# Kernel tuning notes

Measured on AMD Instinct MI355X. Metric: run time of the kernel, lower is better.

The kernel has to match this reference:

```python
import jax, jax.numpy as jnp
import numpy as np

C, H_HEADS, L_LEV, M_PTS = 256, 4, 3, 4
TAU0 = 1.0


def _ln(x, g, b, eps=1e-5):
    mu = x.mean(-1, keepdims=True)
    var = ((x - mu) ** 2).mean(-1, keepdims=True)
    return (x - mu) * jax.lax.rsqrt(var + eps) * g + b


def _grid_sample(v, grid):
    """Bilinear grid_sample, padding_mode='zeros', align_corners=True.
    v: [B,C,Hin,Win], grid: [B,N,2] (x,y) in [-1,1] -> [B,N,C]"""
    B, Cc, Hin, Win = v.shape
    x = (grid[..., 0] + 1.0) * 0.5 * (Win - 1)
    y = (grid[..., 1] + 1.0) * 0.5 * (Hin - 1)
    x0 = jnp.floor(x); y0 = jnp.floor(y)
    wx1 = x - x0; wy1 = y - y0
    x0i = x0.astype(jnp.int32); y0i = y0.astype(jnp.int32)
    vflat = v.reshape(B, Cc, Hin * Win).transpose(0, 2, 1)  # [B,HW,C]

    def tap(yi, xi, w):
        valid = ((xi >= 0) & (xi < Win) & (yi >= 0) & (yi < Hin)).astype(v.dtype)
        idx = jnp.clip(yi, 0, Hin - 1) * Win + jnp.clip(xi, 0, Win - 1)  # [B,N]
        g = jax.vmap(lambda vf, i: vf[i])(vflat, idx)  # [B,N,C]
        return g * (w * valid)[..., None]

    return (tap(y0i, x0i, (1 - wy1) * (1 - wx1))
            + tap(y0i, x0i + 1, (1 - wy1) * wx1)
            + tap(y0i + 1, x0i, wy1 * (1 - wx1))
            + tap(y0i + 1, x0i + 1, wy1 * wx1))


def setup_inputs() -> dict:
    key = jax.random.key(0)
    ks = jax.random.split(key, 32)
    B, Hq, Wq = 2, 64, 64
    cins = [256, 512, 1024]
    d = {
        'S':  jax.random.normal(ks[0], (B, C, Hq, Wq), jnp.float32),
        'f0': jax.random.normal(ks[1], (B, cins[0], 64, 64), jnp.float32),
        'f1': jax.random.normal(ks[2], (B, cins[1], 32, 32), jnp.float32),
        'f2': jax.random.normal(ks[3], (B, cins[2], 16, 16), jnp.float32),
        'sim': jax.random.uniform(ks[4], (B, 1, Hq, Wq), jnp.float32),
        # 1x1 conv value projections per level
        'vw0': jax.random.normal(ks[5], (C, cins[0]), jnp.float32) * 0.02,
        'vb0': jnp.zeros((C,), jnp.float32),
        'vw1': jax.random.normal(ks[6], (C, cins[1]), jnp.float32) * 0.02,
        'vb1': jnp.zeros((C,), jnp.float32),
        'vw2': jax.random.normal(ks[7], (C, cins[2]), jnp.float32) * 0.02,
        'vb2': jnp.zeros((C,), jnp.float32),
        'q_w': jax.random.normal(ks[8], (C, C), jnp.float32) * 0.02,
        'q_b': jnp.zeros((C,), jnp.float32),
        # offset/weight predictors (non-zero so sampling is nontrivial)
        'off_w': jax.random.normal(ks[9], (H_HEADS * L_LEV * M_PTS * 2, C), jnp.float32) * 0.01,
        'off_b': jnp.zeros((H_HEADS * L_LEV * M_PTS * 2,), jnp.float32),
        'wgt_w': jax.random.normal(ks[10], (H_HEADS * L_LEV * M_PTS, C), jnp.float32) * 0.02,
        'wgt_b': jnp.zeros((H_HEADS * L_LEV * M_PTS,), jnp.float32),
        'out_w': jax.random.normal(ks[11], (C, H_HEADS * C), jnp.float32) * 0.02,
        'out_b': jnp.zeros((C,), jnp.float32),
        'lnq_g': jnp.ones((C,), jnp.float32), 'lnq_b': jnp.zeros((C,), jnp.float32),
        'lno_g': jnp.ones((C,), jnp.float32), 'lno_b': jnp.zeros((C,), jnp.float32),
        'fc1_w': jax.random.normal(ks[12], (4 * C, C), jnp.float32) * 0.02,
        'fc1_b': jnp.zeros((4 * C,), jnp.float32),
        'fc2_w': jax.random.normal(ks[13], (C, 4 * C), jnp.float32) * 0.02,
        'fc2_b': jnp.zeros((C,), jnp.float32),
    }
    return d


def reference(S, f0, f1, f2, sim, vw0, vb0, vw1, vb1, vw2, vb2, q_w, q_b,
              off_w, off_b, wgt_w, wgt_b, out_w, out_b,
              lnq_g, lnq_b, lno_g, lno_b, fc1_w, fc1_b, fc2_w, fc2_b):
    B, Cc, Hq, Wq = S.shape
    Nq = Hq * Wq
    S_seq = S.reshape(B, Cc, Nq).transpose(0, 2, 1)  # [B,Nq,C]
    Q = _ln(S_seq @ q_w.T + q_b, lnq_g, lnq_b)

    # reference points in [0,1], (x,y)
    ys = jnp.linspace(0.5 / Hq, 1 - 0.5 / Hq, Hq)
    xs = jnp.linspace(0.5 / Wq, 1 - 0.5 / Wq, Wq)
    yy, xx = jnp.meshgrid(ys, xs, indexing='ij')
    ref = jnp.stack([xx, yy], axis=-1).reshape(1, Nq, 2)

    feats = [(f0, vw0, vb0), (f1, vw1, vb1), (f2, vw2, vb2)]
    V = [jnp.einsum('bchw,oc->bohw', f, w) + b[None, :, None, None] for f, w, b in feats]

    off = (Q @ off_w.T + off_b).reshape(B, Nq, H_HEADS, L_LEV, M_PTS, 2)
    wts = (Q @ wgt_w.T + wgt_b).reshape(B, Nq, H_HEADS, L_LEV, M_PTS)

    sim2 = sim[:, 0].reshape(B, Nq, 1)
    tau = TAU0 / (sim2 + 0.001)
    wts = wts / tau.reshape(B, Nq, 1, 1, 1)
    wts = jax.nn.softmax(wts.reshape(B, Nq, H_HEADS, L_LEV * M_PTS), axis=-1)
    wts = wts.reshape(B, Nq, H_HEADS, L_LEV, M_PTS)

    acc = jnp.zeros((B, Nq, H_HEADS, Cc), S.dtype)
    for l in range(L_LEV):
        g01 = ref.reshape(1, Nq, 1, 1, 2) + off[:, :, :, l]  # [B,Nq,H,M,2]
        g = jnp.clip(jnp.tanh(g01 * 2.0 - 1.0), -1.0, 1.0)
        samp = _grid_sample(V[l], g.reshape(B, Nq * H_HEADS * M_PTS, 2))
        samp = samp.reshape(B, Nq, H_HEADS, M_PTS, Cc)
        acc = acc + jnp.einsum('bqhmc,bqhm->bqhc', samp, wts[:, :, :, l])

    Y = acc.reshape(B, Nq, H_HEADS * Cc) @ out_w.T + out_b
    Z = _ln(S_seq + Y, lno_g, lno_b)
    h = jax.nn.gelu(Z @ fc1_w.T + fc1_b, approximate=False)
    Z = Z + (h @ fc2_w.T + fc2_b)
    return Z.transpose(0, 2, 1).reshape(B, Cc, Hq, Wq)
```

## Files before the change

kernel.cpp:

```cpp
#include <hip/hip_runtime.h>
#include <hip/hip_bf16.h>
#include <math.h>

#define NQ 4096
#define CC 256

typedef __attribute__((ext_vector_type(8))) short bfrag;
typedef __attribute__((ext_vector_type(4))) float ffrag;

__device__ inline unsigned short f2bf(float x) {
  __hip_bfloat16 h = __float2bfloat16(x);
  return *reinterpret_cast<unsigned short*>(&h);
}

__device__ inline float bf2f(unsigned short u) {
  return __uint_as_float(((unsigned)u) << 16);
}

__device__ inline void gload16(const void* g, void* l) {
  __builtin_amdgcn_global_load_lds(
      (const __attribute__((address_space(1))) void*)g,
      (__attribute__((address_space(3))) void*)l, 16, 0, 0);
}

__device__ void tr64(const float* __restrict__ src,
                     unsigned short* __restrict__ dstb, int Cin, int P,
                     int p0, int c0, int b, float (*t)[73]) {
  int tid = threadIdx.x;
  int rx = tid & 15, ry = tid >> 4;
  const float* Sb = src + (size_t)b * Cin * P + p0 + rx * 4;
  #pragma unroll
  for (int i = 0; i < 4; i++) {
    int r = ry + i * 16;
    float4 v = *(const float4*)(Sb + (size_t)(c0 + r) * P);
    t[r][rx * 4 + 0] = v.x; t[r][rx * 4 + 1] = v.y;
    t[r][rx * 4 + 2] = v.z; t[r][rx * 4 + 3] = v.w;
  }
  __syncthreads();
  size_t ob = (size_t)b * P * Cin;
  #pragma unroll
  for (int i = 0; i < 4; i++) {
    int pr = ry + i * 16;
    float x0 = t[rx * 4 + 0][pr], x1 = t[rx * 4 + 1][pr];
    float x2 = t[rx * 4 + 2][pr], x3 = t[rx * 4 + 3][pr];
    size_t idx = ob + (size_t)(p0 + pr) * Cin + c0 + rx * 4;
    ushort4 u4;
    u4.x = f2bf(x0); u4.y = f2bf(x1); u4.z = f2bf(x2); u4.w = f2bf(x3);
    *(ushort4*)(dstb + idx) = u4;
  }
}

__global__ __launch_bounds__(256)
void prep_all_k(const float* S, const float* f0, const float* f1, const float* f2,
                const float* q_w, const float* off_w, const float* wgt_w,
                const float* vw0, const float* vw1, const float* vw2,
                const float* out_w, const float* fc1_w, const float* fc2_w,
                const float* off_b, const float* wgt_b,
                unsigned short* Sbf,
                unsigned short* Xf0, unsigned short* Xf1, unsigned short* Xf2,
                unsigned short* q_wb, unsigned short* owb,
                unsigned short* vw0b, unsigned short* vw1b, unsigned short* vw2b,
                unsigned short* out_wb, unsigned short* fc1_wb,
                unsigned short* fc2_wb, float* bias144) {
  __shared__ float t[64][73];
  int bid = blockIdx.x;
  if (bid < 512) {
    int l = bid;
    tr64(S, Sbf, 256, 4096, (l & 63) * 64, ((l >> 6) & 3) * 64, l >> 8, t);
  } else if (bid < 1024) {
    int l = bid - 512;
    tr64(f0, Xf0, 256, 4096, (l & 63) * 64, ((l >> 6) & 3) * 64, l >> 8, t);
  } else if (bid < 1280) {
    int l = bid - 1024;
    tr64(f1, Xf1, 512, 1024, (l & 15) * 64, ((l >> 4) & 7) * 64, l >> 7, t);
  } else if (bid < 1408) {
    int l = bid - 1280;
    tr64(f2, Xf2, 1024, 256, (l & 3) * 64, ((l >> 2) & 15) * 64, l >> 6, t);
  } else if (bid < 2688) {
    int i4 = (bid - 1408) * 256 + threadIdx.x;
    const float* src; unsigned short* dst;
    if (i4 < 16384)       { src = q_w;   dst = q_wb; }
    else if (i4 < 32768)  { i4 -= 16384;  src = vw0;   dst = vw0b; }
    else if (i4 < 65536)  { i4 -= 32768;  src = vw1;   dst = vw1b; }
    else if (i4 < 131072) { i4 -= 65536;  src = vw2;   dst = vw2b; }
    else if (i4 < 196608) { i4 -= 131072; src = out_w; dst = out_wb; }
    else if (i4 < 262144) { i4 -= 196608; src = fc1_w; dst = fc1_wb; }
    else                  { i4 -= 262144; src = fc2_w; dst = fc2_wb; }
    float4 v = ((const float4*)src)[i4];
    ushort4 u; u.x = f2bf(v.x); u.y = f2bf(v.y); u.z = f2bf(v.z); u.w = f2bf(v.w);
    ((ushort4*)dst)[i4] = u;
  } else {
    int e = (bid - 2688) * 256 + threadIdx.x;
    float v = (e < 24576) ? off_w[e] : (e < 36864 ? wgt_w[e - 24576] : 0.f);
    owb[e] = f2bf(v);
    if (e < 96) bias144[e] = off_b[e];
    else if (e < 144) bias144[e] = wgt_b[e - 96];
  }
}

template<int BM, int BN, int WM, int WN, int EPI>
__device__ __forceinline__ void gemm_body(
    const unsigned short* __restrict__ A, const unsigned short* __restrict__ B,
    const float* __restrict__ bias, float* __restrict__ outf,
    unsigned short* __restrict__ outb, int N, int Kloop, int lda, int ldb,
    int ldo, const unsigned short* __restrict__ Zres, float* __restrict__ outT,
    int m0, int n0, unsigned short* As, unsigned short* Bs) {
  constexpr int MI = BM / (WM * 16), NI = BN / (WN * 16);
  constexpr int TA = BM / 8, TB = BN / 8;
  constexpr int LBM = (BM == 32) ? 5 : (BM == 64) ? 6 : 7;
  constexpr int LBN = (BN == 64) ? 6 : (BN == 128) ? 7 : 8;
  int tid = threadIdx.x, wave = tid >> 6, lane = tid & 63;
  int quad = lane >> 4, l16 = lane & 15;
  int wm = wave / WN, wn = wave % WN;
  const int mbase = wm * (BM / WM), nbase = wn * (BN / WN);

  ffrag acc[MI][NI];
  #pragma unroll
  for (int i = 0; i < MI; i++)
    #pragma unroll
    for (int j = 0; j < NI; j++) acc[i][j] = (ffrag)0.f;

  for (int k0 = 0; k0 < Kloop; k0 += 64) {
    __syncthreads();
    for (int t = wave; t < TA + TB; t += 4) {
      if (t < TA) {
        int s = t * 64 + lane;
        int kc = s >> LBM, r = s & (BM - 1);
        gload16(A + (size_t)(m0 + r) * lda + k0 + kc * 8, (char*)As + t * 1024);
      } else {
        int s = (t - TA) * 64 + lane;
        int kc = s >> LBN, r = s & (BN - 1);
        gload16(B + (size_t)(n0 + r) * ldb + k0 + kc * 8, (char*)Bs + (t - TA) * 1024);
      }
    }
    __syncthreads();
    #pragma unroll
    for (int ks = 0; ks < 2; ks++) {
      bfrag af[MI], bf[NI];
      #pragma unroll
      for (int mi = 0; mi < MI; mi++)
        af[mi] = *(const bfrag*)(As + ((((ks * 4 + quad) << LBM) + mbase + mi * 16 + l16) << 3));
      #pragma unroll
      for (int ni = 0; ni < NI; ni++)
        bf[ni] = *(const bfrag*)(Bs + ((((ks * 4 + quad) << LBN) + nbase + ni * 16 + l16) << 3));
      #pragma unroll
      for (int mi = 0; mi < MI; mi++)
        #pragma unroll
        for (int ni = 0; ni < NI; ni++)
          acc[mi][ni] = __builtin_amdgcn_mfma_f32_16x16x32_bf16(
              af[mi], bf[ni], acc[mi][ni], 0, 0, 0);
    }
  }

  if (EPI == 2) {
    #pragma unroll
    for (int mi = 0; mi < MI; mi++) {
      int mrow = m0 + mbase + mi * 16 + quad * 4;
      int bb = mrow >> 12, q0 = mrow & (NQ - 1);
      #pragma unroll
      for (int ni = 0; ni < NI; ni++) {
        int n = n0 + nbase + ni * 16 + l16;
        float bv = bias[n];
        float4 v;
        v.x = acc[mi][ni][0] + bv + bf2f(Zres[(size_t)(mrow + 0) * CC + n]);
        v.y = acc[mi][ni][1] + bv + bf2f(Zres[(size_t)(mrow + 1) * CC + n]);
        v.z = acc[mi][ni][2] + bv + bf2f(Zres[(size_t)(mrow + 2) * CC + n]);
        v.w = acc[mi][ni][3] + bv + bf2f(Zres[(size_t)(mrow + 3) * CC + n]);
        *(float4*)(outT + ((size_t)(bb * CC + n)) * NQ + q0) = v;
      }
    }
  } else {
    #pragma unroll
    for (int mi = 0; mi < MI; mi++) {
      int mrow = m0 + mbase + mi * 16 + quad * 4;
      #pragma unroll
      for (int ni = 0; ni < NI; ni++) {
        int n = n0 + nbase + ni * 16 + l16;
        if (n < N) {
          float bv = (EPI == 4) ? 0.f : bias[n];
          #pragma unroll
          for (int r = 0; r < 4; r++) {
            float v = acc[mi][ni][r] + bv;
            if (EPI == 1) {
              v = 0.5f * v * (1.f + erff(v * 0.70710678118654752f));
              outb[(size_t)(mrow + r) * ldo + n] = f2bf(v);
            } else if (EPI == 3) {
              outb[(size_t)(mrow + r) * ldo + n] = f2bf(v);
            } else {
              outf[(size_t)(mrow + r) * ldo + n] = v;
            }
          }
        }
      }
    }
  }
}

__device__ __forceinline__ void gemm_ln_q(
    const unsigned short* __restrict__ A, const unsigned short* __restrict__ B,
    const float* __restrict__ bias, unsigned short* __restrict__ outb,
    const float* __restrict__ g, const float* __restrict__ be,
    int m0, char* sm) {
  unsigned short* As = (unsigned short*)sm;
  unsigned short* Bs = (unsigned short*)(sm + 4096);
  float* L = (float*)sm;
  const int K = 256;

  int tid = threadIdx.x, wave = tid >> 6, lane = tid & 63;
  int quad = lane >> 4, l16 = lane & 15;

  ffrag acc[2][4];
  #pragma unroll
  for (int i = 0; i < 2; i++)
    #pragma unroll
    for (int j = 0; j < 4; j++) acc[i][j] = (ffrag)0.f;

  for (int k0 = 0; k0 < K; k0 += 64) {
    __syncthreads();
    for (int t = wave; t < 36; t += 4) {
      if (t < 4) {
        int s = t * 64 + lane;
        int kc = s >> 5, r = s & 31;
        gload16(A + (size_t)(m0 + r) * K + k0 + kc * 8, sm + t * 1024);
      } else {
        int s = (t - 4) * 64 + lane;
        int kc = s >> 8, r = s & 255;
        gload16(B + (size_t)r * K + k0 + kc * 8, sm + 4096 + (t - 4) * 1024);
      }
    }
    __syncthreads();
    #pragma unroll
    for (int ks = 0; ks < 2; ks++) {
      bfrag af[2], bf[4];
      #pragma unroll
      for (int mi = 0; mi < 2; mi++)
        af[mi] = *(const bfrag*)(As + ((((ks * 4 + quad) << 5) + mi * 16 + l16) << 3));
      #pragma unroll
      for (int ni = 0; ni < 4; ni++)
        bf[ni] = *(const bfrag*)(Bs + ((((ks * 4 + quad) << 8) + wave * 64 + ni * 16 + l16) << 3));
      #pragma unroll
      for (int mi = 0; mi < 2; mi++)
        #pragma unroll
        for (int ni = 0; ni < 4; ni++)
          acc[mi][ni] = __builtin_amdgcn_mfma_f32_16x16x32_bf16(
              af[mi], bf[ni], acc[mi][ni], 0, 0, 0);
    }
  }
  __syncthreads();

  #pragma unroll
  for (int mi = 0; mi < 2; mi++) {
    int row = mi * 16 + quad * 4;
    #pragma unroll
    for (int ni = 0; ni < 4; ni++) {
      int col = wave * 64 + ni * 16 + l16;
      float bv = bias[col];
      #pragma unroll
      for (int r = 0; r < 4; r++)
        L[(row + r) * 264 + col] = acc[mi][ni][r] + bv;
    }
  }
  __syncthreads();

  int row = tid >> 3, j = tid & 7;
  int seg = ((j + row) & 7) * 32;
  const float* Lr = L + row * 264 + seg;
  float s1 = 0.f, s2 = 0.f;
  #pragma unroll
  for (int i = 0; i < 8; i++) {
    float4 t4 = *(const float4*)(Lr + i * 4);
    s1 += t4.x + t4.y + t4.z + t4.w;
    s2 += t4.x * t4.x + t4.y * t4.y + t4.z * t4.z + t4.w * t4.w;
  }
  #pragma unroll
  for (int o = 1; o < 8; o <<= 1) {
    s1 += __shfl_xor(s1, o);
    s2 += __shfl_xor(s2, o);
  }
  float mu = s1 * (1.f / 256.f);
  float var = s2 * (1.f / 256.f) - mu * mu;
  float rs = rsqrtf(var + 1e-5f);
  int gm = m0 + row;
  #pragma unroll
  for (int i = 0; i < 8; i++) {
    int col = seg + i * 4;
    float4 t4 = *(const float4*)(Lr + i * 4);
    float4 gg = *(const float4*)(g + col);
    float4 bb4 = *(const float4*)(be + col);
    ushort4 ub;
    ub.x = f2bf((t4.x - mu) * rs * gg.x + bb4.x);
    ub.y = f2bf((t4.y - mu) * rs * gg.y + bb4.y);
    ub.z = f2bf((t4.z - mu) * rs * gg.z + bb4.z);
    ub.w = f2bf((t4.w - mu) * rs * gg.w + bb4.w);
    *(ushort4*)(outb + (size_t)gm * CC + col) = ub;
  }
}

__global__ __launch_bounds__(256)
void qv_k(const unsigned short* Sbf, const unsigned short* q_wb, const float* q_b,
          const float* lnq_g, const float* lnq_b, unsigned short* Qbf,
          const unsigned short* Xf0, const unsigned short* Xf1,
          const unsigned short* Xf2, const unsigned short* vw0b,
          const unsigned short* vw1b, const unsigned short* vw2b,
          const float* vb0, unsigned short* V0b, float* Vp1, float* Vp2) {
  __shared__ __attribute__((aligned(16))) char sm[36864];
  int bid = blockIdx.x;
  unsigned short* As = (unsigned short*)sm;
  unsigned short* Bs = (unsigned short*)(sm + 8192);
  if (bid < 256) {
    gemm_ln_q(Sbf, q_wb, q_b, Qbf, lnq_g, lnq_b, bid * 32, sm);
  } else if (bid < 512) {
    int t = bid - 256;
    gemm_body<64, 128, 2, 2, 3>(Xf0, vw0b, vb0, nullptr, V0b, 256, 256, 256, 256,
                                256, nullptr, nullptr, (t >> 1) * 64, (t & 1) * 128, As, Bs);
  } else if (bid < 640) {
    int l = bid - 512, ks = l >> 6, t = l & 63;
    gemm_body<64, 128, 2, 2, 4>(Xf1 + ks * 256, vw1b + ks * 256, nullptr,
                                Vp1 + (size_t)ks * 524288, nullptr, 256, 256, 512, 512,
                                256, nullptr, nullptr, (t >> 1) * 64, (t & 1) * 128, As, Bs);
  } else {
    int l = bid - 640, ks = l >> 4, t = l & 15;
    gemm_body<64, 128, 2, 2, 4>(Xf2 + ks * 256, vw2b + ks * 256, nullptr,
                                Vp2 + (size_t)ks * 131072, nullptr, 256, 256, 1024, 1024,
                                256, nullptr, nullptr, (t >> 1) * 64, (t & 1) * 128, As, Bs);
  }
}

__global__ __launch_bounds__(256)
void offv_k(const unsigned short* Qbf, const unsigned short* owb,
            const float* bias144, float* offwgt,
            const float* Vp1, const float* Vp2, const float* vb1,
            const float* vb2, unsigned short* V1b, unsigned short* V2b) {
  __shared__ __attribute__((aligned(16))) unsigned short As[4096];
  __shared__ __attribute__((aligned(16))) unsigned short Bs[16384];
  int bid = blockIdx.x;
  if (bid < 128) {
    gemm_body<64, 256, 2, 2, 0>(Qbf, owb, bias144, offwgt, nullptr, 144, 256, 256,
                                256, 144, nullptr, nullptr, bid * 64, 0, As, Bs);
  } else if (bid < 640) {
    int e4 = (bid - 128) * 256 + threadIdx.x;
    const float4* P = (const float4*)Vp1;
    float4 a = P[e4], b = P[e4 + 131072];
    float4 bb = *(const float4*)(vb1 + ((e4 << 2) & 255));
    ushort4 u;
    u.x = f2bf(a.x + b.x + bb.x); u.y = f2bf(a.y + b.y + bb.y);
    u.z = f2bf(a.z + b.z + bb.z); u.w = f2bf(a.w + b.w + bb.w);
    ((ushort4*)V1b)[e4] = u;
  } else {
    int e4 = (bid - 640) * 256 + threadIdx.x;
    const float4* P = (const float4*)Vp2;
    float4 a = P[e4], b = P[e4 + 32768], c = P[e4 + 65536], d = P[e4 + 98304];
    float4 bb = *(const float4*)(vb2 + ((e4 << 2) & 255));
    ushort4 u;
    u.x = f2bf(a.x + b.x + c.x + d.x + bb.x);
    u.y = f2bf(a.y + b.y + c.y + d.y + bb.y);
    u.z = f2bf(a.z + b.z + c.z + d.z + bb.z);
    u.w = f2bf(a.w + b.w + c.w + d.w + bb.w);
    ((ushort4*)V2b)[e4] = u;
  }
}

__global__ __launch_bounds__(256)
void outA_k(const unsigned short* accbf, const unsigned short* out_wb, float* Op) {
  __shared__ __attribute__((aligned(16))) char sm[36864];
  int ks = blockIdx.y;
  gemm_body<32, 256, 1, 4, 4>(accbf + ks * 512, out_wb + ks * 512, nullptr,
                              Op + (size_t)ks * 2097152, nullptr, 256, 512, 1024,
                              1024, 256, nullptr, nullptr, blockIdx.x * 32, 0,
                              (unsigned short*)sm, (unsigned short*)(sm + 4096));
}

__global__ __launch_bounds__(256)
void outB_k(const float* __restrict__ Op, const float* __restrict__ S,
            const float* __restrict__ out_b, const float* __restrict__ g,
            const float* __restrict__ be, unsigned short* __restrict__ Zbf) {
  __shared__ float Ls[16][264];
  int q0 = blockIdx.x * 16;
  int b = q0 >> 12, qq = q0 & (NQ - 1);
  int t = threadIdx.x;
  {
    int cs = t >> 2, j = (t & 3) * 4;
    #pragma unroll
    for (int c0 = 0; c0 < 256; c0 += 64) {
      float4 sv = *(const float4*)(S + (((size_t)(b * 256 + c0 + cs)) << 12) + qq + j);
      Ls[j + 0][c0 + cs] = sv.x; Ls[j + 1][c0 + cs] = sv.y;
      Ls[j + 2][c0 + cs] = sv.z; Ls[j + 3][c0 + cs] = sv.w;
    }
  }
  __syncthreads();
  int c = t;
  float bv = out_b[c];
  float val[16];
  #pragma unroll
  for (int r = 0; r < 16; r++) {
    size_t idx = (size_t)(q0 + r) * 256 + c;
    val[r] = Op[idx] + Op[idx + 2097152] + bv + Ls[r][c];
  }
  __syncthreads();
  #pragma unroll
  for (int r = 0; r < 16; r++) Ls[r][c] = val[r];
  __syncthreads();
  int row = t >> 4, lg = t & 15;
  const float* Lr = &Ls[row][lg * 16];
  float s1 = 0.f, s2 = 0.f;
  #pragma unroll
  for (int i = 0; i < 4; i++) {
    float4 t4 = *(const float4*)(Lr + i * 4);
    s1 += t4.x + t4.y + t4.z + t4.w;
    s2 += t4.x * t4.x + t4.y * t4.y + t4.z * t4.z + t4.w * t4.w;
  }
  #pragma unroll
  for (int o = 1; o < 16; o <<= 1) {
    s1 += __shfl_xor(s1, o);
    s2 += __shfl_xor(s2, o);
  }
  float mu = s1 * (1.f / 256.f);
  float var = s2 * (1.f / 256.f) - mu * mu;
  float rs = rsqrtf(var + 1e-5f);
  int gm = q0 + row;
  #pragma unroll
  for (int i = 0; i < 4; i++) {
    int col = lg * 16 + i * 4;
    float4 t4 = *(const float4*)(Lr + i * 4);
    float4 gg = *(const float4*)(g + col);
    float4 bb4 = *(const float4*)(be + col);
    ushort4 ub;
    ub.x = f2bf((t4.x - mu) * rs * gg.x + bb4.x);
    ub.y = f2bf((t4.y - mu) * rs * gg.y + bb4.y);
    ub.z = f2bf((t4.z - mu) * rs * gg.z + bb4.z);
    ub.w = f2bf((t4.w - mu) * rs * gg.w + bb4.w);
    *(ushort4*)(Zbf + (size_t)gm * CC + col) = ub;
  }
}

__global__ __launch_bounds__(256)
void fc1_k(const unsigned short* Zbf, const unsigned short* fc1_wb,
           const float* fc1_b, unsigned short* hbf) {
  __shared__ __attribute__((aligned(16))) unsigned short As[4096];
  __shared__ __attribute__((aligned(16))) unsigned short Bs[16384];
  gemm_body<64, 256, 2, 2, 1>(Zbf, fc1_wb, fc1_b, nullptr, hbf, 1024, 256, 256,
                              256, 1024, nullptr, nullptr,
                              blockIdx.y * 64, blockIdx.x * 256, As, Bs);
}

__global__ __launch_bounds__(256)
void fc2_k(const unsigned short* hbf, const unsigned short* fc2_wb,
           const float* fc2_b, const unsigned short* Zbf, float* outp) {
  __shared__ __attribute__((aligned(16))) unsigned short As[4096];
  __shared__ __attribute__((aligned(16))) unsigned short Bs[4096];
  gemm_body<64, 64, 2, 2, 2>(hbf, fc2_wb, fc2_b, nullptr, nullptr, 256, 1024,
                             1024, 1024, 256, Zbf, outp,
                             blockIdx.y * 64, blockIdx.x * 64, As, Bs);
}

__global__ __launch_bounds__(256)
void sample_k(const float* __restrict__ ow, const float* __restrict__ sim,
              const unsigned short* __restrict__ V0, const unsigned short* __restrict__ V1,
              const unsigned short* __restrict__ V2, unsigned short* __restrict__ acc) {
  int bn = blockIdx.x;
  int q = ((bn & 7) << 10) | (bn >> 3);
  int b = q >> 12, n = q & (NQ - 1);
  int tid = threadIdx.x, head = tid >> 6, lane = tid & 63;
  int half = lane >> 5, l32 = lane & 31;

  __shared__ float s_w[48];
  __shared__ int   s_xy[48][2];
  __shared__ float s_f[48][2];
  __shared__ uint2 s_ow[192];

  if (tid < 48) {
    int hh = tid / 12, pt = tid % 12, l = pt >> 2, mm = pt & 3;
    int oidx = (hh * 3 + l) * 4 + mm;
    float offx = ow[(size_t)q * 144 + oidx * 2 + 0];
    float offy = ow[(size_t)q * 144 + oidx * 2 + 1];
    float refx = ((n & 63) + 0.5f) * (1.f / 64.f);
    float refy = ((n >> 6) + 0.5f) * (1.f / 64.f);
    float gx = tanhf((refx + offx) * 2.f - 1.f);
    float gy = tanhf((refy + offy) * 2.f - 1.f);
    gx = fminf(1.f, fmaxf(-1.f, gx));
    gy = fminf(1.f, fmaxf(-1.f, gy));
    int Wl = 64 >> l;
    float x = (gx + 1.f) * 0.5f * (float)(Wl - 1);
    float y = (gy + 1.f) * 0.5f * (float)(Wl - 1);
    float x0 = floorf(x), y0 = floorf(y);
    s_xy[tid][0] = (int)x0;
    s_xy[tid][1] = (int)y0;
    s_f[tid][0] = x - x0;
    s_f[tid][1] = y - y0;
    s_w[tid] = ow[(size_t)q * 144 + 96 + oidx] * (sim[q] + 0.001f);
  }
  __syncthreads();
  if (tid < 4) {
    float mx = -1e30f;
    #pragma unroll
    for (int i = 0; i < 12; i++) mx = fmaxf(mx, s_w[tid * 12 + i]);
    float e[12], ssum = 0.f;
    #pragma unroll
    for (int i = 0; i < 12; i++) { e[i] = expf(s_w[tid * 12 + i] - mx); ssum += e[i]; }
    float inv = 1.f / ssum;
    #pragma unroll
    for (int i = 0; i < 12; i++) s_w[tid * 12 + i] = e[i] * inv;
  }
  __syncthreads();
  if (tid < 192) {
    int s = tid >> 2, tap = tid & 3;
    int l = (s % 12) >> 2;
    int Wl = 64 >> l;
    int X = s_xy[s][0] + (tap & 1), Y = s_xy[s][1] + (tap >> 1);
    bool valid = (X >= 0 && X < Wl && Y >= 0 && Y < Wl);
    float wx = (tap & 1) ? s_f[s][0] : 1.f - s_f[s][0];
    float wy = (tap >> 1) ? s_f[s][1] : 1.f - s_f[s][1];
    float twt = valid ? s_w[s] * wx * wy : 0.f;
    int Xc = min(max(X, 0), Wl - 1), Yc = min(max(Y, 0), Wl - 1);
    s_ow[tid].x = (unsigned)((Yc * Wl + Xc) << 8);
    s_ow[tid].y = __float_as_uint(twt);
  }
  __syncthreads();

  const unsigned short* B0 = V0 + (size_t)b * 4096 * CC;
  const unsigned short* B1 = V1 + (size_t)b * 1024 * CC;
  const unsigned short* B2 = V2 + (size_t)b * 256 * CC;
  int ch8 = l32 * 8;
  float a0 = 0.f, a1 = 0.f, a2 = 0.f, a3 = 0.f;
  float a4 = 0.f, a5 = 0.f, a6 = 0.f, a7 = 0.f;
  #pragma unroll
  for (int it = 0; it < 24; it++) {
    const unsigned short* base = (it < 8) ? B0 : (it < 16) ? B1 : B2;
    uint2 owv = s_ow[head * 48 + it * 2 + half];
    float w = __uint_as_float(owv.y);
    const uint4 u = *(const uint4*)(base + owv.x + ch8);
    a0 = fmaf(w, __uint_as_float(u.x << 16), a0);
    a1 = fmaf(w, __uint_as_float(u.x & 0xffff0000u), a1);
    a2 = fmaf(w, __uint_as_float(u.y << 16), a2);
    a3 = fmaf(w, __uint_as_float(u.y & 0xffff0000u), a3);
    a4 = fmaf(w, __uint_as_float(u.z << 16), a4);
    a5 = fmaf(w, __uint_as_float(u.z & 0xffff0000u), a5);
    a6 = fmaf(w, __uint_as_float(u.w << 16), a6);
    a7 = fmaf(w, __uint_as_float(u.w & 0xffff0000u), a7);
  }
  a0 += __shfl_xor(a0, 32); a1 += __shfl_xor(a1, 32);
  a2 += __shfl_xor(a2, 32); a3 += __shfl_xor(a3, 32);
  a4 += __shfl_xor(a4, 32); a5 += __shfl_xor(a5, 32);
  a6 += __shfl_xor(a6, 32); a7 += __shfl_xor(a7, 32);
  if (half == 0) {
    uint4 r;
    r.x = (unsigned)f2bf(a0) | ((unsigned)f2bf(a1) << 16);
    r.y = (unsigned)f2bf(a2) | ((unsigned)f2bf(a3) << 16);
    r.z = (unsigned)f2bf(a4) | ((unsigned)f2bf(a5) << 16);
    r.w = (unsigned)f2bf(a6) | ((unsigned)f2bf(a7) << 16);
    *(uint4*)(acc + (size_t)q * 1024 + head * CC + ch8) = r;
  }
}

extern "C" void kernel_launch(void* const* d_in, const int* in_sizes, int n_in,
                              void* d_out, int out_size, void* d_ws, size_t ws_size,
                              hipStream_t stream) {
  const float* S     = (const float*)d_in[0];
  const float* f0    = (const float*)d_in[1];
  const float* f1    = (const float*)d_in[2];
  const float* f2    = (const float*)d_in[3];
  const float* sim   = (const float*)d_in[4];
  const float* vw0   = (const float*)d_in[5];
  const float* vb0   = (const float*)d_in[6];
  const float* vw1   = (const float*)d_in[7];
  const float* vb1   = (const float*)d_in[8];
  const float* vw2   = (const float*)d_in[9];
  const float* vb2   = (const float*)d_in[10];
  const float* q_w   = (const float*)d_in[11];
  const float* q_b   = (const float*)d_in[12];
  const float* off_w = (const float*)d_in[13];
  const float* off_b = (const float*)d_in[14];
  const float* wgt_w = (const float*)d_in[15];
  const float* wgt_b = (const float*)d_in[16];
  const float* out_w = (const float*)d_in[17];
  const float* out_b = (const float*)d_in[18];
  const float* lnq_g = (const float*)d_in[19];
  const float* lnq_b = (const float*)d_in[20];
  const float* lno_g = (const float*)d_in[21];
  const float* lno_b = (const float*)d_in[22];
  const float* fc1_w = (const float*)d_in[23];
  const float* fc1_b = (const float*)d_in[24];
  const float* fc2_w = (const float*)d_in[25];
  const float* fc2_b = (const float*)d_in[26];

  char* p = (char*)d_ws;
  float* offwgt = (float*)p; p += 4718592;
  float* bias144 = (float*)p; p += 1024;
  float* Pp     = (float*)p; p += 16777216;
  float* Vp1    = (float*)p; p += 4194304;
  float* Vp2    = (float*)p; p += 2097152;
  unsigned short* Sbf   = (unsigned short*)p; p += 4194304;
  unsigned short* Qbf   = (unsigned short*)p; p += 4194304;
  unsigned short* accbf = (unsigned short*)p; p += 16777216;
  unsigned short* V0b   = (unsigned short*)p; p += 4194304;
  unsigned short* V1b   = (unsigned short*)p; p += 1048576;
  unsigned short* V2b   = (unsigned short*)p; p += 262144;
  unsigned short* q_wb   = (unsigned short*)p; p += 131072;
  unsigned short* owb    = (unsigned short*)p; p += 131072;
  unsigned short* vw0b   = (unsigned short*)p; p += 131072;
  unsigned short* vw1b   = (unsigned short*)p; p += 262144;
  unsigned short* vw2b   = (unsigned short*)p; p += 524288;
  unsigned short* out_wb = (unsigned short*)p; p += 524288;
  unsigned short* fc1_wb = (unsigned short*)p; p += 524288;
  unsigned short* fc2_wb = (unsigned short*)p; p += 524288;

  unsigned short* Xf0 = accbf;
  unsigned short* Xf1 = accbf + 2097152;
  unsigned short* Xf2 = accbf + 3145728;
  unsigned short* Zbf = Qbf;
  unsigned short* hbf = accbf;
  float* outp = (float*)d_out;

  prep_all_k<<<2944, 256, 0, stream>>>(S, f0, f1, f2, q_w, off_w, wgt_w,
      vw0, vw1, vw2, out_w, fc1_w, fc2_w, off_b, wgt_b,
      Sbf, Xf0, Xf1, Xf2, q_wb, owb, vw0b, vw1b, vw2b, out_wb,
      fc1_wb, fc2_wb, bias144);

  qv_k<<<704, 256, 0, stream>>>(Sbf, q_wb, q_b, lnq_g, lnq_b, Qbf,
      Xf0, Xf1, Xf2, vw0b, vw1b, vw2b, vb0, V0b, Vp1, Vp2);

  offv_k<<<768, 256, 0, stream>>>(Qbf, owb, bias144, offwgt,
      Vp1, Vp2, vb1, vb2, V1b, V2b);

  sample_k<<<8192, 256, 0, stream>>>(offwgt, sim, V0b, V1b, V2b, accbf);

  outA_k<<<dim3(256, 2), 256, 0, stream>>>(accbf, out_wb, Pp);

  outB_k<<<512, 256, 0, stream>>>(Pp, S, out_b, lno_g, lno_b, Zbf);

  fc1_k<<<dim3(4, 128), 256, 0, stream>>>(Zbf, fc1_wb, fc1_b, hbf);

  fc2_k<<<dim3(4, 128), 256, 0, stream>>>(hbf, fc2_wb, fc2_b, Zbf, outp);
}
```

Measured before the change: 264.7 us.

## Drop split-K partials, fuse out-projection with residual LayerNorm, retile fc2

The V1/V2 projections no longer use split-K with fp32 partial buffers and a separate reduce kernel. Each is now computed in one pass over the full K with bias and bf16 output, and the long-K blocks are scheduled first in qv_k. The out-projection GEMM now runs over the full K=1024 in a new outAB_k kernel that adds bias and residual and applies LayerNorm in its epilogue, which removes the Pp partial round-trip and the outB_k launch. The offset GEMM is retiled to 32-row blocks and fc2 to 64x128 tiles. The cost is fewer blocks and longer K loops per block, so there is less parallelism on the out-projection (256 blocks) and on the V1/V2 GEMMs.

```diff
diff --git a/kernel.cpp b/kernel.cpp
--- a/kernel.cpp
+++ b/kernel.cpp
@@ -302,125 +302,134 @@
           const unsigned short* Xf0, const unsigned short* Xf1,
           const unsigned short* Xf2, const unsigned short* vw0b,
           const unsigned short* vw1b, const unsigned short* vw2b,
-          const float* vb0, unsigned short* V0b, float* Vp1, float* Vp2) {
+          const float* vb0, const float* vb1, const float* vb2,
+          unsigned short* V0b, unsigned short* V1b, unsigned short* V2b) {
   __shared__ __attribute__((aligned(16))) char sm[36864];
   int bid = blockIdx.x;
   unsigned short* As = (unsigned short*)sm;
   unsigned short* Bs = (unsigned short*)(sm + 8192);
-  if (bid < 256) {
-    gemm_ln_q(Sbf, q_wb, q_b, Qbf, lnq_g, lnq_b, bid * 32, sm);
-  } else if (bid < 512) {
-    int t = bid - 256;
-    gemm_body<64, 128, 2, 2, 3>(Xf0, vw0b, vb0, nullptr, V0b, 256, 256, 256, 256,
-                                256, nullptr, nullptr, (t >> 1) * 64, (t & 1) * 128, As, Bs);
-  } else if (bid < 640) {
-    int l = bid - 512, ks = l >> 6, t = l & 63;
-    gemm_body<64, 128, 2, 2, 4>(Xf1 + ks * 256, vw1b + ks * 256, nullptr,
-                                Vp1 + (size_t)ks * 524288, nullptr, 256, 256, 512, 512,
-                                256, nullptr, nullptr, (t >> 1) * 64, (t & 1) * 128, As, Bs);
+  if (bid < 16) {
+    gemm_body<64, 128, 2, 2, 3>(Xf2, vw2b, vb2, nullptr, V2b, 256, 1024, 1024,
+                                1024, 256, nullptr, nullptr, (bid >> 1) * 64,
+                                (bid & 1) * 128, As, Bs);
+  } else if (bid < 80) {
+    int l = bid - 16;
+    gemm_body<64, 128, 2, 2, 3>(Xf1, vw1b, vb1, nullptr, V1b, 256, 512, 512,
+                                512, 256, nullptr, nullptr, (l >> 1) * 64,
+                                (l & 1) * 128, As, Bs);
+  } else if (bid < 336) {
+    int t = bid - 80;
+    gemm_body<64, 128, 2, 2, 3>(Xf0, vw0b, vb0, nullptr, V0b, 256, 256, 256,
+                                256, 256, nullptr, nullptr, (t >> 1) * 64,
+                                (t & 1) * 128, As, Bs);
   } else {
-    int l = bid - 640, ks = l >> 4, t = l & 15;
-    gemm_body<64, 128, 2, 2, 4>(Xf2 + ks * 256, vw2b + ks * 256, nullptr,
-                                Vp2 + (size_t)ks * 131072, nullptr, 256, 256, 1024, 1024,
-                                256, nullptr, nullptr, (t >> 1) * 64, (t & 1) * 128, As, Bs);
+    gemm_ln_q(Sbf, q_wb, q_b, Qbf, lnq_g, lnq_b, (bid - 336) * 32, sm);
   }
 }
 
 __global__ __launch_bounds__(256)
-void offv_k(const unsigned short* Qbf, const unsigned short* owb,
-            const float* bias144, float* offwgt,
-            const float* Vp1, const float* Vp2, const float* vb1,
-            const float* vb2, unsigned short* V1b, unsigned short* V2b) {
-  __shared__ __attribute__((aligned(16))) unsigned short As[4096];
+void offw_k(const unsigned short* Qbf, const unsigned short* owb,
+            const float* bias144, float* offwgt) {
+  __shared__ __attribute__((aligned(16))) unsigned short As[2048];
   __shared__ __attribute__((aligned(16))) unsigned short Bs[16384];
-  int bid = blockIdx.x;
-  if (bid < 128) {
-    gemm_body<64, 256, 2, 2, 0>(Qbf, owb, bias144, offwgt, nullptr, 144, 256, 256,
-                                256, 144, nullptr, nullptr, bid * 64, 0, As, Bs);
-  } else if (bid < 640) {
-    int e4 = (bid - 128) * 256 + threadIdx.x;
-    const float4* P = (const float4*)Vp1;
-    float4 a = P[e4], b = P[e4 + 131072];
-    float4 bb = *(const float4*)(vb1 + ((e4 << 2) & 255));
-    ushort4 u;
-    u.x = f2bf(a.x + b.x + bb.x); u.y = f2bf(a.y + b.y + bb.y);
-    u.z = f2bf(a.z + b.z + bb.z); u.w = f2bf(a.w + b.w + bb.w);
-    ((ushort4*)V1b)[e4] = u;
-  } else {
-    int e4 = (bid - 640) * 256 + threadIdx.x;
-    const float4* P = (const float4*)Vp2;
-    float4 a = P[e4], b = P[e4 + 32768], c = P[e4 + 65536], d = P[e4 + 98304];
-    float4 bb = *(const float4*)(vb2 + ((e4 << 2) & 255));
-    ushort4 u;
-    u.x = f2bf(a.x + b.x + c.x + d.x + bb.x);
-    u.y = f2bf(a.y + b.y + c.y + d.y + bb.y);
-    u.z = f2bf(a.z + b.z + c.z + d.z + bb.z);
-    u.w = f2bf(a.w + b.w + c.w + d.w + bb.w);
-    ((ushort4*)V2b)[e4] = u;
-  }
+  gemm_body<32, 256, 1, 4, 0>(Qbf, owb, bias144, offwgt, nullptr, 144, 256, 256,
+                              256, 144, nullptr, nullptr, blockIdx.x * 32, 0,
+                              As, Bs);
 }
 
 __global__ __launch_bounds__(256)
-void outA_k(const unsigned short* accbf, const unsigned short* out_wb, float* Op) {
+void outAB_k(const unsigned short* __restrict__ A,
+             const unsigned short* __restrict__ Bw,
+             const float* __restrict__ S, const float* __restrict__ out_b,
+             const float* __restrict__ g, const float* __restrict__ be,
+             unsigned short* __restrict__ outb) {
   __shared__ __attribute__((aligned(16))) char sm[36864];
-  int ks = blockIdx.y;
-  gemm_body<32, 256, 1, 4, 4>(accbf + ks * 512, out_wb + ks * 512, nullptr,
-                              Op + (size_t)ks * 2097152, nullptr, 256, 512, 1024,
-                              1024, 256, nullptr, nullptr, blockIdx.x * 32, 0,
-                              (unsigned short*)sm, (unsigned short*)(sm + 4096));
-}
-
-__global__ __launch_bounds__(256)
-void outB_k(const float* __restrict__ Op, const float* __restrict__ S,
-            const float* __restrict__ out_b, const float* __restrict__ g,
-            const float* __restrict__ be, unsigned short* __restrict__ Zbf) {
-  __shared__ float Ls[16][264];
-  int q0 = blockIdx.x * 16;
-  int b = q0 >> 12, qq = q0 & (NQ - 1);
-  int t = threadIdx.x;
-  {
-    int cs = t >> 2, j = (t & 3) * 4;
-    #pragma unroll
-    for (int c0 = 0; c0 < 256; c0 += 64) {
-      float4 sv = *(const float4*)(S + (((size_t)(b * 256 + c0 + cs)) << 12) + qq + j);
-      Ls[j + 0][c0 + cs] = sv.x; Ls[j + 1][c0 + cs] = sv.y;
-      Ls[j + 2][c0 + cs] = sv.z; Ls[j + 3][c0 + cs] = sv.w;
-    }
-  }
-  __syncthreads();
-  int c = t;
-  float bv = out_b[c];
-  float val[16];
-  #pragma unroll
-  for (int r = 0; r < 16; r++) {
-    size_t idx = (size_t)(q0 + r) * 256 + c;
-    val[r] = Op[idx] + Op[idx + 2097152] + bv + Ls[r][c];
-  }
-  __syncthreads();
-  #pragma unroll
-  for (int r = 0; r < 16; r++) Ls[r][c] = val[r];
-  __syncthreads();
-  int row = t >> 4, lg = t & 15;
-  const float* Lr = &Ls[row][lg * 16];
+  unsigned short* As = (unsigned short*)sm;
+  unsigned short* Bs = (unsigned short*)(sm + 4096);
+  float* L = (float*)sm;
+  const int K = 1024;
+  int m0 = blockIdx.x * 32;
+  int tid = threadIdx.x, wave = tid >> 6, lane = tid & 63;
+  int quad = lane >> 4, l16 = lane & 15;
+
+  ffrag acc[2][4];
+  #pragma unroll
+  for (int i = 0; i < 2; i++)
+    #pragma unroll
+    for (int j = 0; j < 4; j++) acc[i][j] = (ffrag)0.f;
+
+  for (int k0 = 0; k0 < K; k0 += 64) {
+    __syncthreads();
+    for (int t = wave; t < 36; t += 4) {
+      if (t < 4) {
+        int s = t * 64 + lane;
+        int kc = s >> 5, r = s & 31;
+        gload16(A + (size_t)(m0 + r) * K + k0 + kc * 8, sm + t * 1024);
+      } else {
+        int s = (t - 4) * 64 + lane;
+        int kc = s >> 8, r = s & 255;
+        gload16(Bw + (size_t)r * K + k0 + kc * 8, sm + 4096 + (t - 4) * 1024);
+      }
+    }
+    __syncthreads();
+    #pragma unroll
+    for (int ks = 0; ks < 2; ks++) {
+      bfrag af[2], bf[4];
+      #pragma unroll
+      for (int mi = 0; mi < 2; mi++)
+        af[mi] = *(const bfrag*)(As + ((((ks * 4 + quad) << 5) + mi * 16 + l16) << 3));
+      #pragma unroll
+      for (int ni = 0; ni < 4; ni++)
+        bf[ni] = *(const bfrag*)(Bs + ((((ks * 4 + quad) << 8) + wave * 64 + ni * 16 + l16) << 3));
+      #pragma unroll
+      for (int mi = 0; mi < 2; mi++)
+        #pragma unroll
+        for (int ni = 0; ni < 4; ni++)
+          acc[mi][ni] = __builtin_amdgcn_mfma_f32_16x16x32_bf16(
+              af[mi], bf[ni], acc[mi][ni], 0, 0, 0);
+    }
+  }
+  __syncthreads();
+
+  int b = m0 >> 12, qq = m0 & (NQ - 1);
+  #pragma unroll
+  for (int mi = 0; mi < 2; mi++) {
+    int row = mi * 16 + quad * 4;
+    #pragma unroll
+    for (int ni = 0; ni < 4; ni++) {
+      int col = wave * 64 + ni * 16 + l16;
+      float bv = out_b[col];
+      float4 sv = *(const float4*)(S + (((size_t)(b * 256 + col)) << 12) + qq + row);
+      L[(row + 0) * 264 + col] = acc[mi][ni][0] + bv + sv.x;
+      L[(row + 1) * 264 + col] = acc[mi][ni][1] + bv + sv.y;
+      L[(row + 2) * 264 + col] = acc[mi][ni][2] + bv + sv.z;
+      L[(row + 3) * 264 + col] = acc[mi][ni][3] + bv + sv.w;
+    }
+  }
+  __syncthreads();
+
+  int row = tid >> 3, j = tid & 7;
+  int seg = ((j + row) & 7) * 32;
+  const float* Lr = L + row * 264 + seg;
   float s1 = 0.f, s2 = 0.f;
   #pragma unroll
-  for (int i = 0; i < 4; i++) {
+  for (int i = 0; i < 8; i++) {
     float4 t4 = *(const float4*)(Lr + i * 4);
     s1 += t4.x + t4.y + t4.z + t4.w;
     s2 += t4.x * t4.x + t4.y * t4.y + t4.z * t4.z + t4.w * t4.w;
   }
   #pragma unroll
-  for (int o = 1; o < 16; o <<= 1) {
+  for (int o = 1; o < 8; o <<= 1) {
     s1 += __shfl_xor(s1, o);
     s2 += __shfl_xor(s2, o);
   }
   float mu = s1 * (1.f / 256.f);
   float var = s2 * (1.f / 256.f) - mu * mu;
   float rs = rsqrtf(var + 1e-5f);
-  int gm = q0 + row;
-  #pragma unroll
-  for (int i = 0; i < 4; i++) {
-    int col = lg * 16 + i * 4;
+  int gm = m0 + row;
+  #pragma unroll
+  for (int i = 0; i < 8; i++) {
+    int col = seg + i * 4;
     float4 t4 = *(const float4*)(Lr + i * 4);
     float4 gg = *(const float4*)(g + col);
     float4 bb4 = *(const float4*)(be + col);
@@ -429,7 +438,7 @@
     ub.y = f2bf((t4.y - mu) * rs * gg.y + bb4.y);
     ub.z = f2bf((t4.z - mu) * rs * gg.z + bb4.z);
     ub.w = f2bf((t4.w - mu) * rs * gg.w + bb4.w);
-    *(ushort4*)(Zbf + (size_t)gm * CC + col) = ub;
+    *(ushort4*)(outb + (size_t)gm * CC + col) = ub;
   }
 }
 
@@ -447,10 +456,10 @@
 void fc2_k(const unsigned short* hbf, const unsigned short* fc2_wb,
            const float* fc2_b, const unsigned short* Zbf, float* outp) {
   __shared__ __attribute__((aligned(16))) unsigned short As[4096];
-  __shared__ __attribute__((aligned(16))) unsigned short Bs[4096];
-  gemm_body<64, 64, 2, 2, 2>(hbf, fc2_wb, fc2_b, nullptr, nullptr, 256, 1024,
-                             1024, 1024, 256, Zbf, outp,
-                             blockIdx.y * 64, blockIdx.x * 64, As, Bs);
+  __shared__ __attribute__((aligned(16))) unsigned short Bs[8192];
+  gemm_body<64, 128, 2, 2, 2>(hbf, fc2_wb, fc2_b, nullptr, nullptr, 256, 1024,
+                              1024, 1024, 256, Zbf, outp,
+                              blockIdx.y * 64, blockIdx.x * 128, As, Bs);
 }
 
 __global__ __launch_bounds__(256)
@@ -586,9 +595,6 @@
   char* p = (char*)d_ws;
   float* offwgt = (float*)p; p += 4718592;
   float* bias144 = (float*)p; p += 1024;
-  float* Pp     = (float*)p; p += 16777216;
-  float* Vp1    = (float*)p; p += 4194304;
-  float* Vp2    = (float*)p; p += 2097152;
   unsigned short* Sbf   = (unsigned short*)p; p += 4194304;
   unsigned short* Qbf   = (unsigned short*)p; p += 4194304;
   unsigned short* accbf = (unsigned short*)p; p += 16777216;
@@ -616,19 +622,16 @@
       Sbf, Xf0, Xf1, Xf2, q_wb, owb, vw0b, vw1b, vw2b, out_wb,
       fc1_wb, fc2_wb, bias144);
 
-  qv_k<<<704, 256, 0, stream>>>(Sbf, q_wb, q_b, lnq_g, lnq_b, Qbf,
-      Xf0, Xf1, Xf2, vw0b, vw1b, vw2b, vb0, V0b, Vp1, Vp2);
-
-  offv_k<<<768, 256, 0, stream>>>(Qbf, owb, bias144, offwgt,
-      Vp1, Vp2, vb1, vb2, V1b, V2b);
+  qv_k<<<592, 256, 0, stream>>>(Sbf, q_wb, q_b, lnq_g, lnq_b, Qbf,
+      Xf0, Xf1, Xf2, vw0b, vw1b, vw2b, vb0, vb1, vb2, V0b, V1b, V2b);
+
+  offw_k<<<256, 256, 0, stream>>>(Qbf, owb, bias144, offwgt);
 
   sample_k<<<8192, 256, 0, stream>>>(offwgt, sim, V0b, V1b, V2b, accbf);
 
-  outA_k<<<dim3(256, 2), 256, 0, stream>>>(accbf, out_wb, Pp);
-
-  outB_k<<<512, 256, 0, stream>>>(Pp, S, out_b, lno_g, lno_b, Zbf);
+  outAB_k<<<256, 256, 0, stream>>>(accbf, out_wb, S, out_b, lno_g, lno_b, Zbf);
 
   fc1_k<<<dim3(4, 128), 256, 0, stream>>>(Zbf, fc1_wb, fc1_b, hbf);
 
-  fc2_k<<<dim3(4, 128), 256, 0, stream>>>(hbf, fc2_wb, fc2_b, Zbf, outp);
-}
+  fc2_k<<<dim3(2, 128), 256, 0, stream>>>(hbf, fc2_wb, fc2_b, Zbf, outp);
+}
```

New measurement: 279.9 us. 1.06x slower.

## Double-buffer LDS tiles in GEMM body and retile outA/fc1 GEMMs

Applied to the files above, without the earlier changes.

Adds a double-buffered path to the shared GEMM routine that prefetches the next K-slice into a second LDS buffer while MFMAs run on the current one, removing one barrier per iteration. The value-projection, outA, fc1 and fc2 GEMMs use it. outA moves from 32x256 to 64x128 tiles and fc1 from 64x256 to 64x128 with twice the blocks. The larger LDS footprint may reduce occupancy.

```diff
diff --git a/kernel.cpp b/kernel.cpp
--- a/kernel.cpp
+++ b/kernel.cpp
@@ -98,7 +98,7 @@
   }
 }
 
-template<int BM, int BN, int WM, int WN, int EPI>
+template<int BM, int BN, int WM, int WN, int EPI, int DB>
 __device__ __forceinline__ void gemm_body(
     const unsigned short* __restrict__ A, const unsigned short* __restrict__ B,
     const float* __restrict__ bias, float* __restrict__ outf,
@@ -109,6 +109,7 @@
   constexpr int TA = BM / 8, TB = BN / 8;
   constexpr int LBM = (BM == 32) ? 5 : (BM == 64) ? 6 : 7;
   constexpr int LBN = (BN == 64) ? 6 : (BN == 128) ? 7 : 8;
+  constexpr int ATILE = TA * 1024, BTILE = TB * 1024;
   int tid = threadIdx.x, wave = tid >> 6, lane = tid & 63;
   int quad = lane >> 4, l16 = lane & 15;
   int wm = wave / WN, wn = wave % WN;
@@ -120,35 +121,90 @@
     #pragma unroll
     for (int j = 0; j < NI; j++) acc[i][j] = (ffrag)0.f;
 
-  for (int k0 = 0; k0 < Kloop; k0 += 64) {
-    __syncthreads();
+  if (DB) {
     for (int t = wave; t < TA + TB; t += 4) {
       if (t < TA) {
         int s = t * 64 + lane;
         int kc = s >> LBM, r = s & (BM - 1);
-        gload16(A + (size_t)(m0 + r) * lda + k0 + kc * 8, (char*)As + t * 1024);
+        gload16(A + (size_t)(m0 + r) * lda + kc * 8, (char*)As + t * 1024);
       } else {
         int s = (t - TA) * 64 + lane;
         int kc = s >> LBN, r = s & (BN - 1);
-        gload16(B + (size_t)(n0 + r) * ldb + k0 + kc * 8, (char*)Bs + (t - TA) * 1024);
+        gload16(B + (size_t)(n0 + r) * ldb + kc * 8, (char*)Bs + (t - TA) * 1024);
       }
     }
     __syncthreads();
-    #pragma unroll
-    for (int ks = 0; ks < 2; ks++) {
-      bfrag af[MI], bf[NI];
-      #pragma unroll
-      for (int mi = 0; mi < MI; mi++)
-        af[mi] = *(const bfrag*)(As + ((((ks * 4 + quad) << LBM) + mbase + mi * 16 + l16) << 3));
-      #pragma unroll
-      for (int ni = 0; ni < NI; ni++)
-        bf[ni] = *(const bfrag*)(Bs + ((((ks * 4 + quad) << LBN) + nbase + ni * 16 + l16) << 3));
-      #pragma unroll
-      for (int mi = 0; mi < MI; mi++)
+    int buf = 0;
+    for (int k0 = 0; k0 < Kloop; k0 += 64) {
+      int kn = k0 + 64;
+      if (kn < Kloop) {
+        int bo = buf ^ 1;
+        for (int t = wave; t < TA + TB; t += 4) {
+          if (t < TA) {
+            int s = t * 64 + lane;
+            int kc = s >> LBM, r = s & (BM - 1);
+            gload16(A + (size_t)(m0 + r) * lda + kn + kc * 8,
+                    (char*)As + bo * ATILE + t * 1024);
+          } else {
+            int s = (t - TA) * 64 + lane;
+            int kc = s >> LBN, r = s & (BN - 1);
+            gload16(B + (size_t)(n0 + r) * ldb + kn + kc * 8,
+                    (char*)Bs + bo * BTILE + (t - TA) * 1024);
+          }
+        }
+      }
+      const unsigned short* Ab = (const unsigned short*)((const char*)As + buf * ATILE);
+      const unsigned short* Bb = (const unsigned short*)((const char*)Bs + buf * BTILE);
+      #pragma unroll
+      for (int ks = 0; ks < 2; ks++) {
+        bfrag af[MI], bf[NI];
+        #pragma unroll
+        for (int mi = 0; mi < MI; mi++)
+          af[mi] = *(const bfrag*)(Ab + ((((ks * 4 + quad) << LBM) + mbase + mi * 16 + l16) << 3));
         #pragma unroll
         for (int ni = 0; ni < NI; ni++)
-          acc[mi][ni] = __builtin_amdgcn_mfma_f32_16x16x32_bf16(
-              af[mi], bf[ni], acc[mi][ni], 0, 0, 0);
+          bf[ni] = *(const bfrag*)(Bb + ((((ks * 4 + quad) << LBN) + nbase + ni * 16 + l16) << 3));
+        #pragma unroll
+        for (int mi = 0; mi < MI; mi++)
+          #pragma unroll
+          for (int ni = 0; ni < NI; ni++)
+            acc[mi][ni] = __builtin_amdgcn_mfma_f32_16x16x32_bf16(
+                af[mi], bf[ni], acc[mi][ni], 0, 0, 0);
+      }
+      __syncthreads();
+      buf ^= 1;
+    }
+  } else {
+    for (int k0 = 0; k0 < Kloop; k0 += 64) {
+      __syncthreads();
+      for (int t = wave; t < TA + TB; t += 4) {
+        if (t < TA) {
+          int s = t * 64 + lane;
+          int kc = s >> LBM, r = s & (BM - 1);
+          gload16(A + (size_t)(m0 + r) * lda + k0 + kc * 8, (char*)As + t * 1024);
+        } else {
+          int s = (t - TA) * 64 + lane;
+          int kc = s >> LBN, r = s & (BN - 1);
+          gload16(B + (size_t)(n0 + r) * ldb + k0 + kc * 8, (char*)Bs + (t - TA) * 1024);
+        }
+      }
+      __syncthreads();
+      #pragma unroll
+      for (int ks = 0; ks < 2; ks++) {
+        bfrag af[MI], bf[NI];
+        #pragma unroll
+        for (int mi = 0; mi < MI; mi++)
+          af[mi] = *(const bfrag*)(As + ((((ks * 4 + quad) << LBM) + mbase + mi * 16 + l16) << 3));
+        #pragma unroll
+        for (int ni = 0; ni < NI; ni++)
+          bf[ni] = *(const bfrag*)(Bs + ((((ks * 4 + quad) << LBN) + nbase + ni * 16 + l16) << 3));
+        #pragma unroll
+        for (int mi = 0; mi < MI; mi++)
+          #pragma unroll
+          for (int ni = 0; ni < NI; ni++)
+            acc[mi][ni] = __builtin_amdgcn_mfma_f32_16x16x32_bf16(
+                af[mi], bf[ni], acc[mi][ni], 0, 0, 0);
+      }
     }
   }
 
@@ -303,26 +359,29 @@
           const unsigned short* Xf2, const unsigned short* vw0b,
           const unsigned short* vw1b, const unsigned short* vw2b,
           const float* vb0, unsigned short* V0b, float* Vp1, float* Vp2) {
-  __shared__ __attribute__((aligned(16))) char sm[36864];
+  __shared__ __attribute__((aligned(16))) char sm[49152];
   int bid = blockIdx.x;
   unsigned short* As = (unsigned short*)sm;
-  unsigned short* Bs = (unsigned short*)(sm + 8192);
+  unsigned short* Bs = (unsigned short*)(sm + 16384);
   if (bid < 256) {
     gemm_ln_q(Sbf, q_wb, q_b, Qbf, lnq_g, lnq_b, bid * 32, sm);
   } else if (bid < 512) {
     int t = bid - 256;
-    gemm_body<64, 128, 2, 2, 3>(Xf0, vw0b, vb0, nullptr, V0b, 256, 256, 256, 256,
-                                256, nullptr, nullptr, (t >> 1) * 64, (t & 1) * 128, As, Bs);
+    gemm_body<64, 128, 2, 2, 3, 1>(Xf0, vw0b, vb0, nullptr, V0b, 256, 256, 256,
+                                   256, 256, nullptr, nullptr, (t >> 1) * 64,
+                                   (t & 1) * 128, As, Bs);
   } else if (bid < 640) {
     int l = bid - 512, ks = l >> 6, t = l & 63;
-    gemm_body<64, 128, 2, 2, 4>(Xf1 + ks * 256, vw1b + ks * 256, nullptr,
-                                Vp1 + (size_t)ks * 524288, nullptr, 256, 256, 512, 512,
-                                256, nullptr, nullptr, (t >> 1) * 64, (t & 1) * 128, As, Bs);
+    gemm_body<64, 128, 2, 2, 4, 1>(Xf1 + ks * 256, vw1b + ks * 256, nullptr,
+                                   Vp1 + (size_t)ks * 524288, nullptr, 256, 256,
+                                   512, 512, 256, nullptr, nullptr,
+                                   (t >> 1) * 64, (t & 1) * 128, As, Bs);
   } else {
     int l = bid - 640, ks = l >> 4, t = l & 15;
-    gemm_body<64, 128, 2, 2, 4>(Xf2 + ks * 256, vw2b + ks * 256, nullptr,
-                                Vp2 + (size_t)ks * 131072, nullptr, 256, 256, 1024, 1024,
-                                256, nullptr, nullptr, (t >> 1) * 64, (t & 1) * 128, As, Bs);
+    gemm_body<64, 128, 2, 2, 4, 1>(Xf2 + ks * 256, vw2b + ks * 256, nullptr,
+                                   Vp2 + (size_t)ks * 131072, nullptr, 256, 256,
+                                   1024, 1024, 256, nullptr, nullptr,
+                                   (t >> 1) * 64, (t & 1) * 128, As, Bs);
   }
 }
 
@@ -335,8 +394,9 @@
   __shared__ __attribute__((aligned(16))) unsigned short Bs[16384];
   int bid = blockIdx.x;
   if (bid < 128) {
-    gemm_body<64, 256, 2, 2, 0>(Qbf, owb, bias144, offwgt, nullptr, 144, 256, 256,
-                                256, 144, nullptr, nullptr, bid * 64, 0, As, Bs);
+    gemm_body<64, 256, 2, 2, 0, 0>(Qbf, owb, bias144, offwgt, nullptr, 144, 256,
+                                   256, 256, 144, nullptr, nullptr, bid * 64, 0,
+                                   As, Bs);
   } else if (bid < 640) {
     int e4 = (bid - 128) * 256 + threadIdx.x;
     const float4* P = (const float4*)Vp1;
@@ -362,12 +422,13 @@
 
 __global__ __launch_bounds__(256)
 void outA_k(const unsigned short* accbf, const unsigned short* out_wb, float* Op) {
-  __shared__ __attribute__((aligned(16))) char sm[36864];
-  int ks = blockIdx.y;
-  gemm_body<32, 256, 1, 4, 4>(accbf + ks * 512, out_wb + ks * 512, nullptr,
-                              Op + (size_t)ks * 2097152, nullptr, 256, 512, 1024,
-                              1024, 256, nullptr, nullptr, blockIdx.x * 32, 0,
-                              (unsigned short*)sm, (unsigned short*)(sm + 4096));
+  __shared__ __attribute__((aligned(16))) char sm[49152];
+  int ks = blockIdx.y, bx = blockIdx.x;
+  gemm_body<64, 128, 2, 2, 4, 1>(accbf + ks * 512, out_wb + ks * 512, nullptr,
+                                 Op + (size_t)ks * 2097152, nullptr, 256, 512,
+                                 1024, 1024, 256, nullptr, nullptr,
+                                 (bx >> 1) * 64, (bx & 1) * 128,
+                                 (unsigned short*)sm, (unsigned short*)(sm + 16384));
 }
 
 __global__ __launch_bounds__(256)
@@ -436,21 +497,21 @@
 __global__ __launch_bounds__(256)
 void fc1_k(const unsigned short* Zbf, const unsigned short* fc1_wb,
            const float* fc1_b, unsigned short* hbf) {
-  __shared__ __attribute__((aligned(16))) unsigned short As[4096];
-  __shared__ __attribute__((aligned(16))) unsigned short Bs[16384];
-  gemm_body<64, 256, 2, 2, 1>(Zbf, fc1_wb, fc1_b, nullptr, hbf, 1024, 256, 256,
-                              256, 1024, nullptr, nullptr,
-                              blockIdx.y * 64, blockIdx.x * 256, As, Bs);
+  __shared__ __attribute__((aligned(16))) char sm[49152];
+  gemm_body<64, 128, 2, 2, 1, 1>(Zbf, fc1_wb, fc1_b, nullptr, hbf, 1024, 256,
+                                 256, 256, 1024, nullptr, nullptr,
+                                 blockIdx.y * 64, blockIdx.x * 128,
+                                 (unsigned short*)sm, (unsigned short*)(sm + 16384));
 }
 
 __global__ __launch_bounds__(256)
 void fc2_k(const unsigned short* hbf, const unsigned short* fc2_wb,
            const float* fc2_b, const unsigned short* Zbf, float* outp) {
-  __shared__ __attribute__((aligned(16))) unsigned short As[4096];
-  __shared__ __attribute__((aligned(16))) unsigned short Bs[4096];
-  gemm_body<64, 64, 2, 2, 2>(hbf, fc2_wb, fc2_b, nullptr, nullptr, 256, 1024,
-                             1024, 1024, 256, Zbf, outp,
-                             blockIdx.y * 64, blockIdx.x * 64, As, Bs);
+  __shared__ __attribute__((aligned(16))) char sm[32768];
+  gemm_body<64, 64, 2, 2, 2, 1>(hbf, fc2_wb, fc2_b, nullptr, nullptr, 256, 1024,
+                                1024, 1024, 256, Zbf, outp,
+                                blockIdx.y * 64, blockIdx.x * 64,
+                                (unsigned short*)sm, (unsigned short*)(sm + 16384));
 }
 
 __global__ __launch_bounds__(256)
@@ -628,7 +689,7 @@
 
   outB_k<<<512, 256, 0, stream>>>(Pp, S, out_b, lno_g, lno_b, Zbf);
 
-  fc1_k<<<dim3(4, 128), 256, 0, stream>>>(Zbf, fc1_wb, fc1_b, hbf);
+  fc1_k<<<dim3(8, 128), 256, 0, stream>>>(Zbf, fc1_wb, fc1_b, hbf);
 
   fc2_k<<<dim3(4, 128), 256, 0, stream>>>(hbf, fc2_wb, fc2_b, Zbf, outp);
 }
```

Measured after the change: 253.4 us. -4.3%, faster.
